# Kernel tuning notes

Hardware: AMD Instinct MI355X
Metric: run time of the kernel (lower is better)

The kernel has to match this reference:

```python
import jax, jax.numpy as jnp
import numpy as np

MARGIN = 0.3
N = 8192
D = 128
NUM_CLASSES = 256

def setup_inputs() -> dict:
    key = jax.random.key(0)
    k1, k2 = jax.random.split(key)
    inputs = jax.random.normal(k1, (N, D), dtype=jnp.float32)
    targets = jax.random.randint(k2, (N,), 0, NUM_CLASSES, dtype=jnp.int64)
    return {"inputs": inputs, "targets": targets}

def reference(inputs, targets):
    n = inputs.shape[0]
    dt = inputs.dtype
    # pairwise euclidean distances: ||xi||^2 + ||xj||^2 - 2 xi.xj, clamped and sqrt'ed
    sq = jnp.sum(inputs * inputs, axis=1)                     # [n]
    d2 = sq[:, None] + sq[None, :] - 2.0 * (inputs @ inputs.T)
    dist = jnp.sqrt(jnp.clip(d2, 1e-12, None))                # [n, n]
    dsq = dist * dist                                         # squared dists used by the loss

    mask = targets[:, None] == targets[None, :]               # same-identity mask [n, n]

    # positives: torch code sorts and drops the smallest (the self-distance ~1e-6)
    pos_d = jnp.where(mask, dist, jnp.inf)
    min_idx = jnp.argmin(pos_d, axis=1)                       # index of dropped element per row
    excl = jnp.arange(n)[None, :] == min_idx[:, None]
    pos_valid = mask & ~excl                                  # remaining positives
    cnt_p = jnp.sum(pos_valid, axis=1).astype(dt)
    sigma_p = jnp.sum(jnp.where(pos_valid, dsq, 0.0), axis=1) / cnt_p
    max_p = jnp.max(jnp.where(pos_valid, dsq, -jnp.inf), axis=1)
    dist_ap = max_p / sigma_p + 0.5 * jnp.log(sigma_p)        # [n]

    # negatives: all different-identity entries
    neg = ~mask
    cnt_n = jnp.sum(neg, axis=1).astype(dt)
    sigma_n = jnp.sum(jnp.where(neg, dsq, 0.0), axis=1) / cnt_n
    min_n = jnp.min(jnp.where(neg, dsq, jnp.inf), axis=1)
    dist_an = min_n / sigma_n + 0.5 * jnp.log(sigma_n)        # [n]

    # MarginRankingLoss with y=1: mean(max(0, -(an - ap) + margin))
    loss = jnp.mean(jnp.maximum(dist_ap - dist_an + MARGIN, 0.0))
    return loss
```

## Files before the change

kernel.cpp:

```cpp
#include <hip/hip_runtime.h>
#include <math.h>


#define NROWS 8192
#define MARGIN_F 0.3f

typedef short bf16x8 __attribute__((ext_vector_type(8)));
typedef float f32x16 __attribute__((ext_vector_type(16)));
union U4B { uint4 u; bf16x8 h; };

__device__ __forceinline__ unsigned short f2bf(float x) {
    unsigned u = __float_as_uint(x);
    return (unsigned short)((u + 0x7fffu + ((u >> 16) & 1u)) >> 16);
}

__global__ __launch_bounds__(256) void prep_kernel(const float* __restrict__ X,
                                                   const int* __restrict__ tgt,
                                                   float* __restrict__ sq,
                                                   float* __restrict__ upk,
                                                   unsigned short* __restrict__ Xbf,
                                                   int* __restrict__ hist,
                                                   float* __restrict__ S_class,
                                                   float* __restrict__ bsum) {
    int tid = threadIdx.x, w = tid >> 6, l = tid & 63;
    int row0 = blockIdx.x * 32 + w * 8;
    float rs = 0.0f;
    #pragma unroll
    for (int i = 0; i < 8; ++i) {
        int r = row0 + i;
        float2 v = ((const float2*)X)[(size_t)r * 64 + l];
        ushort2 h2;
        h2.x = f2bf(v.x);
        h2.y = f2bf(v.y);
        ((ushort2*)Xbf)[(size_t)r * 64 + l] = h2;
        float s = v.x * v.x + v.y * v.y;
        for (int d = 32; d > 0; d >>= 1) s += __shfl_down(s, d, 64);
        if (l == 0) {
            sq[r] = s;
            rs += s;
            int c = tgt[r];
            upk[r] = __uint_as_float((__float_as_uint(0.5f * s) & 0xffffff00u) | (unsigned)c);
            atomicAdd(&hist[c], 1);
            atomicAdd(&S_class[c], s);
        }
    }
    __shared__ float bs[4];
    if (l == 0) bs[w] = rs;
    __syncthreads();
    if (tid == 0) bsum[blockIdx.x] = bs[0] + bs[1] + bs[2] + bs[3];
}

__global__ __launch_bounds__(256, 3) void dist_kernel(
        const unsigned short* __restrict__ Xbf, const int* __restrict__ tgt,
        const float* __restrict__ upk, float4* __restrict__ partial,
        int ns_mask, int jb_shift, int tiles) {
    __shared__ uint4 As[128 * 16];
    __shared__ float ush[128];
    const int tid = threadIdx.x;
    const int w = tid >> 6, l = tid & 63, hl = l >> 5, l31 = l & 31;
    const int bx = blockIdx.x;
    const int slice = bx & ns_mask;
    const int jb = bx >> jb_shift;

    {
        const uint4* src = (const uint4*)Xbf + (size_t)jb * 64 * 16;
        #pragma unroll
        for (int s = 0; s < 4; ++s) {
            int g = s * 256 + tid, row = g >> 4, c = g & 15;
            As[row * 16 + (c ^ (row & 15))] = src[g];
        }
    }
    __syncthreads();
    bf16x8 Bf[2][8];
    int tjt[2];
    #pragma unroll
    for (int ct = 0; ct < 2; ++ct) {
        int colb = ct * 32 + l31;
        tjt[ct] = tgt[jb * 64 + colb];
        #pragma unroll
        for (int kk = 0; kk < 8; ++kk) {
            U4B t; t.u = As[colb * 16 + ((kk * 2 + hl) ^ (colb & 15))];
            Bf[ct][kk] = t.h;
        }
    }

    float Sa[2] = {0.f, 0.f};
    float Ss[2] = {0.f, 0.f};
    float Mp[2] = {-INFINITY, -INFINITY};
    float Mn[2] = { INFINITY,  INFINITY};

    for (int t = 0; t < tiles; ++t) {
        const int i0 = (slice * tiles + t) * 128;
        __syncthreads();
        {
            const uint4* src = (const uint4*)Xbf + (size_t)i0 * 16;
            #pragma unroll
            for (int s = 0; s < 8; ++s) {
                int g = s * 256 + tid, row = g >> 4, c = g & 15;
                As[row * 16 + (c ^ (row & 15))] = src[g];
            }
            if (tid < 128) ush[tid] = upk[i0 + tid];
        }
        __syncthreads();

        float ur[16];
        #pragma unroll
        for (int r = 0; r < 16; ++r)
            ur[r] = ush[w * 32 + (r & 3) + 8 * (r >> 2) + 4 * hl];

        f32x16 acc[2];
        acc[0] = (f32x16)0.0f;
        acc[1] = (f32x16)0.0f;
        const int arow = w * 32 + l31;
        #pragma unroll
        for (int kk = 0; kk < 8; ++kk) {
            U4B a; a.u = As[arow * 16 + ((kk * 2 + hl) ^ (arow & 15))];
            acc[0] = __builtin_amdgcn_mfma_f32_32x32x16_bf16(a.h, Bf[0][kk], acc[0], 0, 0, 0);
            acc[1] = __builtin_amdgcn_mfma_f32_32x32x16_bf16(a.h, Bf[1][kk], acc[1], 0, 0, 0);
        }

        #pragma unroll
        for (int ct = 0; ct < 2; ++ct) {
            const int tt = tjt[ct];
            #pragma unroll
            for (int r = 0; r < 16; ++r) {
                float a = acc[ct][r];
                float v = ur[r] - a;
                bool same = ((__float_as_int(ur[r]) & 0xff) == tt);
                Sa[ct] += a;
                Ss[ct] += same ? a : 0.0f;
                Mp[ct] = fmaxf(Mp[ct], same ? v : -INFINITY);
                Mn[ct] = same ? Mn[ct] : fminf(Mn[ct], v);
            }
        }
    }

    #pragma unroll
    for (int ct = 0; ct < 2; ++ct) {
        Sa[ct] += __shfl_xor(Sa[ct], 32, 64);
        Ss[ct] += __shfl_xor(Ss[ct], 32, 64);
        Mp[ct] = fmaxf(Mp[ct], __shfl_xor(Mp[ct], 32, 64));
        Mn[ct] = fminf(Mn[ct], __shfl_xor(Mn[ct], 32, 64));
    }
    __syncthreads();
    float4* sm = (float4*)As;
    if (l < 32) {
        #pragma unroll
        for (int ct = 0; ct < 2; ++ct)
            sm[(ct * 32 + l31) * 4 + w] = make_float4(Sa[ct], Ss[ct], Mp[ct], Mn[ct]);
    }
    __syncthreads();
    if (tid < 64) {
        float4 a = sm[tid * 4 + 0], b = sm[tid * 4 + 1];
        float4 c2 = sm[tid * 4 + 2], d = sm[tid * 4 + 3];
        float4 o;
        o.x = a.x + b.x + c2.x + d.x;
        o.y = a.y + b.y + c2.y + d.y;
        o.z = fmaxf(fmaxf(a.z, b.z), fmaxf(c2.z, d.z));
        o.w = fminf(fminf(a.w, b.w), fminf(c2.w, d.w));
        partial[(size_t)slice * NROWS + jb * 64 + tid] = o;
    }
}

__global__ __launch_bounds__(256) void combine_kernel(
        const float* __restrict__ sq, const int* __restrict__ tgt,
        const int* __restrict__ hist, const float* __restrict__ S_class,
        const float* __restrict__ bsum, const float4* __restrict__ partial,
        float* __restrict__ blocksum, int ns) {
    __shared__ float red[4];
    __shared__ float hs[4];
    int tid = threadIdx.x, l = tid & 63, w = tid >> 6;

    float b = bsum[tid];
    for (int d = 32; d > 0; d >>= 1) b += __shfl_down(b, d, 64);
    if (l == 0) red[w] = b;
    __syncthreads();
    float S_all = red[0] + red[1] + red[2] + red[3];

    int j = blockIdx.x * 256 + tid;
    float Sa = 0.f, Ss = 0.f, Mp = -INFINITY, Mn = INFINITY;
    for (int s = 0; s < ns; ++s) {
        float4 p = partial[(size_t)s * NROWS + j];
        Sa += p.x; Ss += p.y;
        Mp = fmaxf(Mp, p.z); Mn = fminf(Mn, p.w);
    }
    float sqj = sq[j];
    int c = tgt[j];
    float cnt = (float)hist[c];
    float sumall = (float)NROWS * sqj + S_all - 2.0f * Sa;
    float sump = cnt * sqj + S_class[c] - 2.0f * Ss;
    float sumn = sumall - sump;
    float sigp = sump / (cnt - 1.0f);
    float sign_ = sumn / ((float)NROWS - cnt);
    float ap = (sqj + 2.0f * Mp) / sigp + 0.5f * __logf(sigp);
    float an = (sqj + 2.0f * Mn) / sign_ + 0.5f * __logf(sign_);
    float h = fmaxf(ap - an + MARGIN_F, 0.0f);
    for (int d = 32; d > 0; d >>= 1) h += __shfl_down(h, d, 64);
    if (l == 0) hs[w] = h;
    __syncthreads();
    if (tid == 0) blocksum[blockIdx.x] = hs[0] + hs[1] + hs[2] + hs[3];
}

__global__ __launch_bounds__(64) void final_kernel(const float* __restrict__ blocksum,
                                                   float* __restrict__ out) {
    int tid = threadIdx.x;
    float s = (tid < 32) ? blocksum[tid] : 0.0f;
    for (int d = 32; d > 0; d >>= 1) s += __shfl_down(s, d, 64);
    if (tid == 0) out[0] = s * (1.0f / NROWS);
}

extern "C" void kernel_launch(void* const* d_in, const int* in_sizes, int n_in,
                              void* d_out, int out_size, void* d_ws, size_t ws_size,
                              hipStream_t stream) {
    const float* X = (const float*)d_in[0];
    const int* tgt = (const int*)d_in[1];
    float* out = (float*)d_out;

    float* f = (float*)d_ws;
    int*   hist     = (int*)f;
    float* S_class  = f + 256;
    float* bsum     = f + 512;
    float* blocksum = f + 768;
    float* sq       = f + 1024;
    float* upk      = f + 9216;
    unsigned short* Xbf = (unsigned short*)(f + 17408);
    float4* partial = (float4*)(f + 541696);

    int ns = 16;
    while (ns > 2 && ws_size < ((size_t)541696 + (size_t)ns * NROWS * 4) * sizeof(float))
        ns >>= 1;
    int shift = (ns == 16) ? 4 : (ns == 8) ? 3 : 2;
    int tiles = 64 / ns;

    hipMemsetAsync(d_ws, 0, 2048, stream);
    prep_kernel<<<256, 256, 0, stream>>>(X, tgt, sq, upk, Xbf, hist, S_class, bsum);
    dist_kernel<<<128 * ns, 256, 0, stream>>>(Xbf, tgt, upk, partial,
                                              ns - 1, shift, tiles);
    combine_kernel<<<32, 256, 0, stream>>>(sq, tgt, hist, S_class, bsum,
                                           partial, blocksum, ns);
    final_kernel<<<1, 64, 0, stream>>>(blocksum, out);
}
```

Baseline: 119.9 us.

## Fuse prep, distance and combine into one cooperative kernel with grid syncs

```diff
diff --git a/kernel.cpp b/kernel.cpp
--- a/kernel.cpp
+++ b/kernel.cpp
@@ -1,9 +1,17 @@
 #include <hip/hip_runtime.h>
+#include <hip/hip_cooperative_groups.h>
 #include <math.h>
+
+namespace cg = cooperative_groups;
 
 
 #define NROWS 8192
 #define MARGIN_F 0.3f
+
+#define OFF_SQ   0
+#define OFF_UPK  8192
+#define OFF_XBF  16384
+#define OFF_PART 278528
 
 typedef short bf16x8 __attribute__((ext_vector_type(8)));
 typedef float f32x16 __attribute__((ext_vector_type(16)));
@@ -14,20 +22,16 @@
     return (unsigned short)((u + 0x7fffu + ((u >> 16) & 1u)) >> 16);
 }
 
-__global__ __launch_bounds__(256) void prep_kernel(const float* __restrict__ X,
-                                                   const int* __restrict__ tgt,
-                                                   float* __restrict__ sq,
-                                                   float* __restrict__ upk,
-                                                   unsigned short* __restrict__ Xbf,
-                                                   int* __restrict__ hist,
-                                                   float* __restrict__ S_class,
-                                                   float* __restrict__ bsum) {
+__device__ __forceinline__ void phase_prep(int bx, const float* __restrict__ X,
+                                           const int* __restrict__ tgt,
+                                           float* __restrict__ sq,
+                                           float* __restrict__ upk,
+                                           unsigned short* __restrict__ Xbf,
+                                           float* __restrict__ out) {
     int tid = threadIdx.x, w = tid >> 6, l = tid & 63;
-    int row0 = blockIdx.x * 32 + w * 8;
-    float rs = 0.0f;
-    #pragma unroll
-    for (int i = 0; i < 8; ++i) {
-        int r = row0 + i;
+    #pragma unroll
+    for (int i = 0; i < 4; ++i) {
+        int r = bx * 16 + w * 4 + i;
         float2 v = ((const float2*)X)[(size_t)r * 64 + l];
         ushort2 h2;
         h2.x = f2bf(v.x);
@@ -37,30 +41,24 @@
         for (int d = 32; d > 0; d >>= 1) s += __shfl_down(s, d, 64);
         if (l == 0) {
             sq[r] = s;
-            rs += s;
-            int c = tgt[r];
-            upk[r] = __uint_as_float((__float_as_uint(0.5f * s) & 0xffffff00u) | (unsigned)c);
-            atomicAdd(&hist[c], 1);
-            atomicAdd(&S_class[c], s);
-        }
-    }
-    __shared__ float bs[4];
-    if (l == 0) bs[w] = rs;
-    __syncthreads();
-    if (tid == 0) bsum[blockIdx.x] = bs[0] + bs[1] + bs[2] + bs[3];
-}
-
-__global__ __launch_bounds__(256, 3) void dist_kernel(
-        const unsigned short* __restrict__ Xbf, const int* __restrict__ tgt,
-        const float* __restrict__ upk, float4* __restrict__ partial,
-        int ns_mask, int jb_shift, int tiles) {
+            upk[r] = __uint_as_float((__float_as_uint(0.5f * s) & 0xffffff00u)
+                                     | (unsigned)tgt[r]);
+        }
+    }
+    if (bx == 0 && tid == 0) out[0] = 0.0f;
+}
+
+__device__ __forceinline__ void phase_dist(int bx,
+                                           const unsigned short* __restrict__ Xbf,
+                                           const int* __restrict__ tgt,
+                                           const float* __restrict__ upk,
+                                           float4* __restrict__ partial) {
     __shared__ uint4 As[128 * 16];
     __shared__ float ush[128];
     const int tid = threadIdx.x;
     const int w = tid >> 6, l = tid & 63, hl = l >> 5, l31 = l & 31;
-    const int bx = blockIdx.x;
-    const int slice = bx & ns_mask;
-    const int jb = bx >> jb_shift;
+    const int slice = bx & 3;
+    const int jb = bx >> 2;
 
     {
         const uint4* src = (const uint4*)Xbf + (size_t)jb * 64 * 16;
@@ -89,8 +87,8 @@
     float Mp[2] = {-INFINITY, -INFINITY};
     float Mn[2] = { INFINITY,  INFINITY};
 
-    for (int t = 0; t < tiles; ++t) {
-        const int i0 = (slice * tiles + t) * 128;
+    for (int t = 0; t < 16; ++t) {
+        const int i0 = slice * 2048 + t * 128;
         __syncthreads();
         {
             const uint4* src = (const uint4*)Xbf + (size_t)i0 * 16;
@@ -104,9 +102,12 @@
         __syncthreads();
 
         float ur[16];
-        #pragma unroll
-        for (int r = 0; r < 16; ++r)
+        int tags[16];
+        #pragma unroll
+        for (int r = 0; r < 16; ++r) {
             ur[r] = ush[w * 32 + (r & 3) + 8 * (r >> 2) + 4 * hl];
+            tags[r] = __float_as_int(ur[r]) & 0xff;
+        }
 
         f32x16 acc[2];
         acc[0] = (f32x16)0.0f;
@@ -126,7 +127,7 @@
             for (int r = 0; r < 16; ++r) {
                 float a = acc[ct][r];
                 float v = ur[r] - a;
-                bool same = ((__float_as_int(ur[r]) & 0xff) == tt);
+                bool same = (tags[r] == tt);
                 Sa[ct] += a;
                 Ss[ct] += same ? a : 0.0f;
                 Mp[ct] = fmaxf(Mp[ct], same ? v : -INFINITY);
@@ -162,51 +163,93 @@
     }
 }
 
-__global__ __launch_bounds__(256) void combine_kernel(
-        const float* __restrict__ sq, const int* __restrict__ tgt,
-        const int* __restrict__ hist, const float* __restrict__ S_class,
-        const float* __restrict__ bsum, const float4* __restrict__ partial,
-        float* __restrict__ blocksum, int ns) {
+__device__ __forceinline__ void phase_combine(int bx, const int* __restrict__ tgt,
+                                              const float* __restrict__ sq,
+                                              const float4* __restrict__ partial,
+                                              float* __restrict__ out) {
+    __shared__ float scl[256];
+    __shared__ int cnt[256];
     __shared__ float red[4];
     __shared__ float hs[4];
-    int tid = threadIdx.x, l = tid & 63, w = tid >> 6;
-
-    float b = bsum[tid];
-    for (int d = 32; d > 0; d >>= 1) b += __shfl_down(b, d, 64);
-    if (l == 0) red[w] = b;
+    int tid = threadIdx.x, w = tid >> 6, l = tid & 63;
+    scl[tid] = 0.0f;
+    cnt[tid] = 0;
+    __syncthreads();
+    for (int it = 0; it < 32; ++it) {
+        int r = it * 256 + tid;
+        int c = tgt[r];
+        atomicAdd(&scl[c], sq[r]);
+        atomicAdd(&cnt[c], 1);
+    }
+    __syncthreads();
+    float s = scl[tid];
+    for (int d = 32; d > 0; d >>= 1) s += __shfl_down(s, d, 64);
+    if (l == 0) red[w] = s;
     __syncthreads();
     float S_all = red[0] + red[1] + red[2] + red[3];
 
-    int j = blockIdx.x * 256 + tid;
+    int j = bx * 256 + tid;
     float Sa = 0.f, Ss = 0.f, Mp = -INFINITY, Mn = INFINITY;
-    for (int s = 0; s < ns; ++s) {
-        float4 p = partial[(size_t)s * NROWS + j];
+    #pragma unroll
+    for (int s2 = 0; s2 < 4; ++s2) {
+        float4 p = partial[(size_t)s2 * NROWS + j];
         Sa += p.x; Ss += p.y;
         Mp = fmaxf(Mp, p.z); Mn = fminf(Mn, p.w);
     }
     float sqj = sq[j];
     int c = tgt[j];
-    float cnt = (float)hist[c];
+    float cm = (float)cnt[c];
     float sumall = (float)NROWS * sqj + S_all - 2.0f * Sa;
-    float sump = cnt * sqj + S_class[c] - 2.0f * Ss;
+    float sump = cm * sqj + scl[c] - 2.0f * Ss;
     float sumn = sumall - sump;
-    float sigp = sump / (cnt - 1.0f);
-    float sign_ = sumn / ((float)NROWS - cnt);
+    float sigp = sump / (cm - 1.0f);
+    float sign_ = sumn / ((float)NROWS - cm);
     float ap = (sqj + 2.0f * Mp) / sigp + 0.5f * __logf(sigp);
     float an = (sqj + 2.0f * Mn) / sign_ + 0.5f * __logf(sign_);
     float h = fmaxf(ap - an + MARGIN_F, 0.0f);
     for (int d = 32; d > 0; d >>= 1) h += __shfl_down(h, d, 64);
     if (l == 0) hs[w] = h;
     __syncthreads();
-    if (tid == 0) blocksum[blockIdx.x] = hs[0] + hs[1] + hs[2] + hs[3];
-}
-
-__global__ __launch_bounds__(64) void final_kernel(const float* __restrict__ blocksum,
-                                                   float* __restrict__ out) {
-    int tid = threadIdx.x;
-    float s = (tid < 32) ? blocksum[tid] : 0.0f;
-    for (int d = 32; d > 0; d >>= 1) s += __shfl_down(s, d, 64);
-    if (tid == 0) out[0] = s * (1.0f / NROWS);
+    if (tid == 0)
+        atomicAdd(out, (hs[0] + hs[1] + hs[2] + hs[3]) * (1.0f / NROWS));
+}
+
+__global__ __launch_bounds__(256, 2) void fused_kernel(
+        const float* __restrict__ X, const int* __restrict__ tgt,
+        float* __restrict__ f, float* __restrict__ out) {
+    float* sq  = f + OFF_SQ;
+    float* upk = f + OFF_UPK;
+    unsigned short* Xbf = (unsigned short*)(f + OFF_XBF);
+    float4* partial = (float4*)(f + OFF_PART);
+
+    phase_prep(blockIdx.x, X, tgt, sq, upk, Xbf, out);
+    cg::this_grid().sync();
+    phase_dist(blockIdx.x, Xbf, tgt, upk, partial);
+    cg::this_grid().sync();
+    if (blockIdx.x < 32) phase_combine(blockIdx.x, tgt, sq, partial, out);
+}
+
+__global__ __launch_bounds__(256, 2) void prep_k(const float* __restrict__ X,
+                                                 const int* __restrict__ tgt,
+                                                 float* __restrict__ sq,
+                                                 float* __restrict__ upk,
+                                                 unsigned short* __restrict__ Xbf,
+                                                 float* __restrict__ out) {
+    phase_prep(blockIdx.x, X, tgt, sq, upk, Xbf, out);
+}
+
+__global__ __launch_bounds__(256, 2) void dist_k(const unsigned short* __restrict__ Xbf,
+                                                 const int* __restrict__ tgt,
+                                                 const float* __restrict__ upk,
+                                                 float4* __restrict__ partial) {
+    phase_dist(blockIdx.x, Xbf, tgt, upk, partial);
+}
+
+__global__ __launch_bounds__(256) void combine_k(const int* __restrict__ tgt,
+                                                 const float* __restrict__ sq,
+                                                 const float4* __restrict__ partial,
+                                                 float* __restrict__ out) {
+    phase_combine(blockIdx.x, tgt, sq, partial, out);
 }
 
 extern "C" void kernel_launch(void* const* d_in, const int* in_sizes, int n_in,
@@ -215,28 +258,19 @@
     const float* X = (const float*)d_in[0];
     const int* tgt = (const int*)d_in[1];
     float* out = (float*)d_out;
-
     float* f = (float*)d_ws;
-    int*   hist     = (int*)f;
-    float* S_class  = f + 256;
-    float* bsum     = f + 512;
-    float* blocksum = f + 768;
-    float* sq       = f + 1024;
-    float* upk      = f + 9216;
-    unsigned short* Xbf = (unsigned short*)(f + 17408);
-    float4* partial = (float4*)(f + 541696);
-
-    int ns = 16;
-    while (ns > 2 && ws_size < ((size_t)541696 + (size_t)ns * NROWS * 4) * sizeof(float))
-        ns >>= 1;
-    int shift = (ns == 16) ? 4 : (ns == 8) ? 3 : 2;
-    int tiles = 64 / ns;
-
-    hipMemsetAsync(d_ws, 0, 2048, stream);
-    prep_kernel<<<256, 256, 0, stream>>>(X, tgt, sq, upk, Xbf, hist, S_class, bsum);
-    dist_kernel<<<128 * ns, 256, 0, stream>>>(Xbf, tgt, upk, partial,
-                                              ns - 1, shift, tiles);
-    combine_kernel<<<32, 256, 0, stream>>>(sq, tgt, hist, S_class, bsum,
-                                           partial, blocksum, ns);
-    final_kernel<<<1, 64, 0, stream>>>(blocksum, out);
-}
+
+    void* args[] = { (void*)&X, (void*)&tgt, (void*)&f, (void*)&out };
+    hipError_t e = hipLaunchCooperativeKernel((const void*)fused_kernel,
+                                              dim3(512), dim3(256), args, 0, stream);
+    if (e != hipSuccess) {
+        (void)hipGetLastError();
+        float* sq  = f + OFF_SQ;
+        float* upk = f + OFF_UPK;
+        unsigned short* Xbf = (unsigned short*)(f + OFF_XBF);
+        float4* partial = (float4*)(f + OFF_PART);
+        prep_k<<<512, 256, 0, stream>>>(X, tgt, sq, upk, Xbf, out);
+        dist_k<<<512, 256, 0, stream>>>(Xbf, tgt, upk, partial);
+        combine_k<<<32, 256, 0, stream>>>(tgt, sq, partial, out);
+    }
+}
```

Result: slower. 244.6 us (+104.0%).
